# Kernel tuning notes

Measured on AMD Instinct MI355X. Metric: run time of the kernel, lower is better.

## Reference

```python
import jax, jax.numpy as jnp
import numpy as np

B, S, D, H = 2, 2048, 1024, 16
HD = D // H  # head_dim = 64


def setup_inputs() -> dict:
    key = jax.random.key(0)
    ks = jax.random.split(key, 12)
    sc = 1.0 / np.sqrt(D)
    return {
        "query": jax.random.normal(ks[0], (B, S, D), jnp.float32),
        "key_": jax.random.normal(ks[1], (B, S, D), jnp.float32),
        "value": jax.random.normal(ks[2], (B, S, D), jnp.float32),
        "mask": jax.random.randint(ks[3], (B, 1, S, S), 0, 2, jnp.int32),
        "Wq": jax.random.normal(ks[4], (D, D), jnp.float32) * sc,
        "bq": jnp.zeros((D,), jnp.float32),
        "Wk": jax.random.normal(ks[5], (D, D), jnp.float32) * sc,
        "bk": jnp.zeros((D,), jnp.float32),
        "Wv": jax.random.normal(ks[6], (D, D), jnp.float32) * sc,
        "bv": jnp.zeros((D,), jnp.float32),
        "Wo": jax.random.normal(ks[7], (D, D), jnp.float32) * sc,
        "bo": jnp.zeros((D,), jnp.float32),
    }


def _split(x):
    # [B, S, D] -> [B, H, S, HD]
    return x.reshape(B, S, H, HD).transpose(0, 2, 1, 3)


def reference(query, key_, value, mask, Wq, bq, Wk, bk, Wv, bv, Wo, bo):
    Q = _split(query @ Wq + bq)
    K = _split(key_ @ Wk + bk)
    V = _split(value @ Wv + bv)
    # scores: [B, H, Sq, Sk]
    scores = jnp.einsum("bhqd,bhkd->bhqk", Q, K) / jnp.sqrt(jnp.float32(HD))
    scores = jnp.where(mask == 0, jnp.float32(-1e9), scores)
    probs = jax.nn.softmax(scores, axis=-1)
    attn = jnp.einsum("bhqk,bhkd->bhqd", probs, V)
    out = attn.transpose(0, 2, 1, 3).reshape(B, S, D)
    return out @ Wo + bo
```

## Files before the change

kernel.cpp:

```cpp
#include <hip/hip_runtime.h>
#include <stdint.h>

typedef _Float16 f16;
typedef _Float16 f16x4 __attribute__((ext_vector_type(4)));
typedef _Float16 f16x8 __attribute__((ext_vector_type(8)));
typedef __fp16 hf16x2 __attribute__((ext_vector_type(2)));
typedef float f32x4 __attribute__((ext_vector_type(4)));
typedef float f32x16 __attribute__((ext_vector_type(16)));
typedef unsigned u32;
typedef unsigned uint2v __attribute__((ext_vector_type(2)));

static constexpr int Bb = 2, Ss = 2048, Dd = 1024, Hh = 16, HDd = 64;
static constexpr int M_ROWS = Bb * Ss;

static constexpr size_t OFF_WT  = 24ull << 20;
static constexpr size_t OFF_QKV = 32ull << 20;
static constexpr size_t OFF_ATT = 56ull << 20;
static constexpr size_t OFF_MB  = 64ull << 20;

__device__ __forceinline__ void gll16(const void* g, void* l) {
  __builtin_amdgcn_global_load_lds((__attribute__((address_space(1))) const void*)g,
                                   (__attribute__((address_space(3))) void*)l, 16, 0, 0);
}

__device__ __forceinline__ int lds_byte(int row, int slot) {
  return row * 128 + (((slot ^ (row & 7)) & 7) << 4);
}

__device__ __forceinline__ float ex2(float x) {
  float r; asm("v_exp_f32 %0, %1" : "=v"(r) : "v"(x)); return r;
}

union H2U { hf16x2 h; u32 u; };

__global__ __launch_bounds__(256) void prep(const int* __restrict__ mask,
                                            unsigned* __restrict__ bits,
                                            const float* __restrict__ wq,
                                            const float* __restrict__ wk,
                                            const float* __restrict__ wv,
                                            const float* __restrict__ wo,
                                            f16* __restrict__ wt) {
  const int bid = blockIdx.x;
  __shared__ float t[32][33];
  if (bid < 32768) {
    size_t i = (size_t)bid * 256 + threadIdx.x;
    int v = mask[i];
    unsigned long long bm = __ballot(v != 0);
    if ((threadIdx.x & 63) == 0) {
      size_t w = i >> 5;
      bits[w]     = (unsigned)bm;
      bits[w + 1] = (unsigned)(bm >> 32);
    }
  } else {
    const int wb = bid - 32768;
    const int z = wb >> 10, by = (wb >> 5) & 31, bx = wb & 31;
    const float* W = z == 0 ? wq : z == 1 ? wk : z == 2 ? wv : wo;
    f16* Wt = wt + (size_t)z * Dd * Dd;
    const int tx = threadIdx.x & 31, ty = threadIdx.x >> 5;
    const int k0 = by * 32, n0 = bx * 32;
    for (int i = 0; i < 32; i += 8) t[ty + i][tx] = W[(size_t)(k0 + ty + i) * Dd + n0 + tx];
    __syncthreads();
    for (int i = 0; i < 32; i += 8) Wt[(size_t)(n0 + ty + i) * Dd + k0 + tx] = (f16)t[tx][ty + i];
  }
}

__global__ __launch_bounds__(256) void gemm_qkv(const float* __restrict__ qin,
                                                const float* __restrict__ kin,
                                                const float* __restrict__ vin,
                                                const f16* __restrict__ Btbase,
                                                const float* __restrict__ b0,
                                                const float* __restrict__ b1,
                                                const float* __restrict__ b2,
                                                f16* __restrict__ Cbase) {
  constexpr int K = Dd, N = Dd;
  const int f = blockIdx.x;
  const int z = f >> 8, i = f & 255;
  const int xg = i & 7, sl = i >> 3;
  const int m0 = (xg * 4 + (sl >> 3)) * 128, n0 = (sl & 7) * 128;
  const float* A = z == 0 ? qin : z == 1 ? kin : vin;
  const f16* Bt = Btbase + (size_t)z * N * K;
  const float* bias = z == 0 ? b0 : z == 1 ? b1 : b2;

  __shared__ char smem[65536];
  const int tid = threadIdx.x, l = tid & 63, w = tid >> 6;
  const int li = l & 15, gq = l >> 4;
  const int wm = (w >> 1) * 64, wn = (w & 1) * 64;
  const int sr = l >> 3, ss = l & 7;
  const int scol = ((ss ^ sr) << 3);

  f32x4 acc[4][4];
  for (int mi = 0; mi < 4; mi++)
    for (int ni = 0; ni < 4; ni++) acc[mi][ni] = f32x4{0.f, 0.f, 0.f, 0.f};

  float4 a0[4], a1[4];
#pragma unroll
  for (int c = 0; c < 4; c++) {
    int chunk = w * 4 + c, r = chunk * 8 + sr;
    gll16(Bt + (size_t)(n0 + r) * K + scol, smem + 16384 + chunk * 1024);
    const float* src = A + (size_t)(m0 + r) * K + scol;
    a0[c] = *(const float4*)src; a1[c] = *(const float4*)(src + 4);
  }
#pragma unroll
  for (int c = 0; c < 4; c++) {
    int chunk = w * 4 + c;
    H2U h0, h1, h2, h3;
    h0.h = __builtin_amdgcn_cvt_pkrtz(a0[c].x, a0[c].y);
    h1.h = __builtin_amdgcn_cvt_pkrtz(a0[c].z, a0[c].w);
    h2.h = __builtin_amdgcn_cvt_pkrtz(a1[c].x, a1[c].y);
    h3.h = __builtin_amdgcn_cvt_pkrtz(a1[c].z, a1[c].w);
    union { u32 uu[4]; f16x8 v8; } pk;
    pk.uu[0] = h0.u; pk.uu[1] = h1.u; pk.uu[2] = h2.u; pk.uu[3] = h3.u;
    *(f16x8*)(smem + chunk * 1024 + l * 16) = pk.v8;
  }

  int cur = 0;
  for (int it = 0; it < 16; it++) {
    __syncthreads();
    char* Asc = smem + cur * 32768;
    char* Bsc = Asc + 16384;
    char* Asn = smem + (cur ^ 1) * 32768;
    char* Bsn = Asn + 16384;
    if (it < 15) {
      const int kn = (it + 1) * 64;
#pragma unroll
      for (int c = 0; c < 4; c++) {
        int chunk = w * 4 + c, r = chunk * 8 + sr;
        gll16(Bt + (size_t)(n0 + r) * K + kn + scol, Bsn + chunk * 1024);
        const float* src = A + (size_t)(m0 + r) * K + kn + scol;
        a0[c] = *(const float4*)src; a1[c] = *(const float4*)(src + 4);
      }
    }
#pragma unroll
    for (int ks = 0; ks < 2; ks++) {
      f16x8 af[4], bf[4];
#pragma unroll
      for (int ii = 0; ii < 4; ii++) {
        af[ii] = *(const f16x8*)(Asc + lds_byte(wm + ii * 16 + li, ks * 4 + gq));
        bf[ii] = *(const f16x8*)(Bsc + lds_byte(wn + ii * 16 + li, ks * 4 + gq));
      }
#pragma unroll
      for (int mi = 0; mi < 4; mi++)
#pragma unroll
        for (int ni = 0; ni < 4; ni++)
          acc[mi][ni] = __builtin_amdgcn_mfma_f32_16x16x32_f16(af[mi], bf[ni], acc[mi][ni], 0, 0, 0);
    }
    if (it < 15) {
#pragma unroll
      for (int c = 0; c < 4; c++) {
        int chunk = w * 4 + c;
        H2U h0, h1, h2, h3;
        h0.h = __builtin_amdgcn_cvt_pkrtz(a0[c].x, a0[c].y);
        h1.h = __builtin_amdgcn_cvt_pkrtz(a0[c].z, a0[c].w);
        h2.h = __builtin_amdgcn_cvt_pkrtz(a1[c].x, a1[c].y);
        h3.h = __builtin_amdgcn_cvt_pkrtz(a1[c].z, a1[c].w);
        union { u32 uu[4]; f16x8 v8; } pk;
        pk.uu[0] = h0.u; pk.uu[1] = h1.u; pk.uu[2] = h2.u; pk.uu[3] = h3.u;
        *(f16x8*)(Asn + chunk * 1024 + l * 16) = pk.v8;
      }
    }
    cur ^= 1;
  }

  const float scl = (z == 0) ? 0.18033688011112042f : 1.0f;
  if (z == 2) {
    f16* Vt = Cbase + (size_t)2 * M_ROWS * N;
#pragma unroll
    for (int mi = 0; mi < 4; mi++)
#pragma unroll
      for (int ni = 0; ni < 4; ni++) {
        const int col = n0 + wn + ni * 16 + li;
        const int r0  = m0 + wm + mi * 16 + gq * 4;
        const int bb_ = r0 >> 11, s = r0 & 2047;
        const float bv = bias[col];
        f16x4 pk;
#pragma unroll
        for (int j = 0; j < 4; j++) pk[j] = (f16)(acc[mi][ni][j] + bv);
        *(f16x4*)(Vt + ((size_t)(bb_ * Hh) << 17) + (size_t)col * Ss + s) = pk;
      }
  } else {
    for (int mi = 0; mi < 4; mi++)
      for (int ni = 0; ni < 4; ni++) {
        const int r0  = m0 + wm + mi * 16 + gq * 4;
        const int col = n0 + wn + ni * 16 + li;
        const float bb = bias[col];
#pragma unroll
        for (int j = 0; j < 4; j++) {
          float val = (acc[mi][ni][j] + bb) * scl;
          Cbase[(size_t)z * M_ROWS * N + (size_t)(r0 + j) * N + col] = (f16)val;
        }
      }
  }
}

__global__ __launch_bounds__(256) void gemm_out(const f16* __restrict__ A,
                                                const f16* __restrict__ Bt,
                                                const float* __restrict__ bias,
                                                float* __restrict__ C) {
  constexpr int K = Dd, N = Dd;
  const int f = blockIdx.x;
  const int xg = f & 7, sl = f >> 3;
  const int m0 = (xg * 4 + (sl >> 3)) * 128, n0 = (sl & 7) * 128;
  __shared__ char smem[65536];
  const int tid = threadIdx.x, l = tid & 63, w = tid >> 6;
  const int li = l & 15, gq = l >> 4;
  const int wm = (w >> 1) * 64, wn = (w & 1) * 64;
  const int sr = l >> 3, ss = l & 7;
  const int scol = ((ss ^ sr) << 3);

  f32x4 acc[4][4];
  for (int mi = 0; mi < 4; mi++)
    for (int ni = 0; ni < 4; ni++) acc[mi][ni] = f32x4{0.f, 0.f, 0.f, 0.f};

#pragma unroll
  for (int c = 0; c < 4; c++) {
    int chunk = w * 4 + c, r = chunk * 8 + sr;
    gll16(A  + (size_t)(m0 + r) * K + scol, smem + chunk * 1024);
    gll16(Bt + (size_t)(n0 + r) * K + scol, smem + 16384 + chunk * 1024);
  }

  int cur = 0;
  for (int it = 0; it < 16; it++) {
    __syncthreads();
    char* Asc = smem + cur * 32768;
    char* Bsc = Asc + 16384;
    if (it < 15) {
      char* Asn = smem + (cur ^ 1) * 32768;
      const int kn = (it + 1) * 64;
#pragma unroll
      for (int c = 0; c < 4; c++) {
        int chunk = w * 4 + c, r = chunk * 8 + sr;
        gll16(A  + (size_t)(m0 + r) * K + kn + scol, Asn + chunk * 1024);
        gll16(Bt + (size_t)(n0 + r) * K + kn + scol, Asn + 16384 + chunk * 1024);
      }
    }
#pragma unroll
    for (int ks = 0; ks < 2; ks++) {
      f16x8 af[4], bf[4];
#pragma unroll
      for (int ii = 0; ii < 4; ii++) {
        af[ii] = *(const f16x8*)(Asc + lds_byte(wm + ii * 16 + li, ks * 4 + gq));
        bf[ii] = *(const f16x8*)(Bsc + lds_byte(wn + ii * 16 + li, ks * 4 + gq));
      }
#pragma unroll
      for (int mi = 0; mi < 4; mi++)
#pragma unroll
        for (int ni = 0; ni < 4; ni++)
          acc[mi][ni] = __builtin_amdgcn_mfma_f32_16x16x32_f16(af[mi], bf[ni], acc[mi][ni], 0, 0, 0);
    }
    cur ^= 1;
  }

  for (int mi = 0; mi < 4; mi++)
    for (int ni = 0; ni < 4; ni++) {
      const int r0  = m0 + wm + mi * 16 + gq * 4;
      const int col = n0 + wn + ni * 16 + li;
      const float bb = bias[col];
#pragma unroll
      for (int j = 0; j < 4; j++)
        C[(size_t)(r0 + j) * N + col] = acc[mi][ni][j] + bb;
    }
}

__global__ __launch_bounds__(512, 4) void attn_fused(const f16* __restrict__ Qp,
                                                     const f16* __restrict__ Kp,
                                                     const f16* __restrict__ Vt,
                                                     const u32* __restrict__ mbits,
                                                     f16* __restrict__ outp) {
  const int flat = blockIdx.x;
  const int xcd = flat & 7, jj = flat >> 3;
  const int qt = jj & 15;
  const int hb = xcd * 4 + (jj >> 4);
  const int h = hb & 15, b = hb >> 4;

  const int tid = threadIdx.x, l = tid & 63, w = tid >> 6;
  const int lo = l & 31, hi = l >> 5;
  const int half = w >> 2, wsub = w & 3;
  const int q0 = qt * 128, wq = wsub * 32;

  __shared__ char smem[65536];
  char* hbase = smem + half * 32768;
  char* Qst = smem + 16384;

  const size_t qkbase = (size_t)b * Ss * Dd + (size_t)h * HDd;
  const f16* Vtb = Vt + (size_t)(b * Hh + h) * HDd * Ss;
  const int sr = l >> 3, ss = l & 7;
  const int scol = ((ss ^ sr) << 3);

  for (int c = 0; c < 2; c++) {
    int chunk = w * 2 + c, r = chunk * 8 + sr;
    gll16(Qp + qkbase + (size_t)(q0 + r) * Dd + scol, Qst + chunk * 1024);
  }
  const int kt0 = half * 16;
  for (int c = 0; c < 2; c++) {
    int chunk = wsub * 2 + c, r = chunk * 8 + sr;
    gll16(Kp + qkbase + (size_t)(kt0 * 64 + r) * Dd + scol, hbase + chunk * 1024);
    gll16(Vtb + (size_t)r * Ss + kt0 * 64 + scol, hbase + 8192 + chunk * 1024);
  }
  __syncthreads();

  f16x8 qf[4];
#pragma unroll
  for (int c = 0; c < 4; c++)
    qf[c] = *(const f16x8*)(Qst + lds_byte(wq + lo, 2 * c + hi));
  __syncthreads();

  f32x16 accO0 = {0}, accO1 = {0};
  float m_run = -1e30f, l_run = 0.f;
  const u32* mrow = mbits + (size_t)(b * Ss + q0 + wq + lo) * 64;

  for (int it = 0; it < 16; it++) {
    const int kt = kt0 + it;
    if (it) __syncthreads();
    char* bufc = hbase + (it & 1) * 16384;
    if (it < 15) {
      char* bufn = hbase + ((it + 1) & 1) * 16384;
      const int k0n = (kt + 1) * 64;
      for (int c = 0; c < 2; c++) {
        int chunk = wsub * 2 + c, r = chunk * 8 + sr;
        gll16(Kp + qkbase + (size_t)(k0n + r) * Dd + scol, bufn + chunk * 1024);
        gll16(Vtb + (size_t)r * Ss + k0n + scol, bufn + 8192 + chunk * 1024);
      }
    }
    const char* Kb = bufc;
    const char* Vb = bufc + 8192;

    f32x16 s0 = {0}, s1 = {0};
    __builtin_amdgcn_s_setprio(1);
#pragma unroll
    for (int c = 0; c < 4; c++) {
      f16x8 kf0 = *(const f16x8*)(Kb + lds_byte(lo, 2 * c + hi));
      f16x8 kf1 = *(const f16x8*)(Kb + lds_byte(32 + lo, 2 * c + hi));
      s0 = __builtin_amdgcn_mfma_f32_32x32x16_f16(kf0, qf[c], s0, 0, 0, 0);
      s1 = __builtin_amdgcn_mfma_f32_32x32x16_f16(kf1, qf[c], s1, 0, 0, 0);
    }
    __builtin_amdgcn_s_setprio(0);

    uint2v mw = *(const uint2v*)(mrow + kt * 2);
    u32 wa = mw.x >> (hi << 2);
    u32 wb = mw.y >> (hi << 2);

    float x0 = fmaxf(s0[0], s1[0]), x1 = fmaxf(s0[1], s1[1]);
    float x2 = fmaxf(s0[2], s1[2]), x3 = fmaxf(s0[3], s1[3]);
#pragma unroll
    for (int r = 4; r < 16; r += 4) {
      x0 = fmaxf(x0, fmaxf(s0[r],     s1[r]));
      x1 = fmaxf(x1, fmaxf(s0[r + 1], s1[r + 1]));
      x2 = fmaxf(x2, fmaxf(s0[r + 2], s1[r + 2]));
      x3 = fmaxf(x3, fmaxf(s0[r + 3], s1[r + 3]));
    }
    float pm = fmaxf(fmaxf(x0, x1), fmaxf(x2, x3));

    float mn;
    if (__all(pm <= m_run + 11.5f)) {
      mn = m_run;
    } else {
      pm = fmaxf(pm, __shfl_xor(pm, 32));
      mn = fmaxf(m_run, pm);
      const float so = ex2(m_run - mn);
      m_run = mn;
      l_run *= so;
      accO0 *= so; accO1 *= so;
    }

    float racc = 0.f;
#pragma unroll
    for (int r = 0; r < 16; r++) {
      const int kk = (r & 3) + 8 * (r >> 2);
      u32 ma = (u32)(((int)(wa << (31 - kk))) >> 31);
      u32 mb = (u32)(((int)(wb << (31 - kk))) >> 31);
      float e0 = __uint_as_float(__float_as_uint(ex2(s0[r] - mn)) & ma);
      float e1 = __uint_as_float(__float_as_uint(ex2(s1[r] - mn)) & mb);
      s0[r] = e0; s1[r] = e1;
      racc += e0 + e1;
    }
    l_run += racc;

    u32 pw[16];
#pragma unroll
    for (int j = 0; j < 8; j++) {
      H2U a, c;
      a.h = __builtin_amdgcn_cvt_pkrtz(s0[2 * j], s0[2 * j + 1]);
      c.h = __builtin_amdgcn_cvt_pkrtz(s1[2 * j], s1[2 * j + 1]);
      pw[j] = a.u; pw[8 + j] = c.u;
    }
#pragma unroll
    for (int c = 0; c < 4; c++) {
      asm volatile("v_permlane32_swap_b32 %0, %1" : "+v"(pw[4 * c]), "+v"(pw[4 * c + 2]));
      asm volatile("v_permlane32_swap_b32 %0, %1" : "+v"(pw[4 * c + 1]), "+v"(pw[4 * c + 3]));
    }

    __builtin_amdgcn_s_setprio(1);
#pragma unroll
    for (int c = 0; c < 4; c++) {
      union { u32 u[4]; f16x8 v; } pu;
      pu.u[0] = pw[4 * c]; pu.u[1] = pw[4 * c + 1];
      pu.u[2] = pw[4 * c + 2]; pu.u[3] = pw[4 * c + 3];
      f16x8 vf0 = *(const f16x8*)(Vb + lds_byte(lo, 2 * c + hi));
      f16x8 vf1 = *(const f16x8*)(Vb + lds_byte(32 + lo, 2 * c + hi));
      accO0 = __builtin_amdgcn_mfma_f32_32x32x16_f16(vf0, pu.v, accO0, 0, 0, 0);
      accO1 = __builtin_amdgcn_mfma_f32_32x32x16_f16(vf1, pu.v, accO1, 0, 0, 0);
    }
    __builtin_amdgcn_s_setprio(0);
  }

  __syncthreads();
  float* mg = (float*)smem;
  if (half == 1) {
    float* p = mg + (size_t)(wsub * 64 + l) * 35;
#pragma unroll
    for (int r = 0; r < 16; r++) { p[r] = accO0[r]; p[16 + r] = accO1[r]; }
    p[32] = m_run; p[33] = l_run;
  }
  __syncthreads();
  if (half == 1) return;

  const float* p = mg + (size_t)(wsub * 64 + l) * 35;
  const float mB = p[32], lB = p[33];
  const float m = fmaxf(m_run, mB);
  const float fA = ex2(m_run - m), fB = ex2(mB - m);
  float lmerged = l_run * fA + lB * fB;
#pragma unroll
  for (int r = 0; r < 16; r++) {
    accO0[r] = accO0[r] * fA + p[r] * fB;
    accO1[r] = accO1[r] * fA + p[16 + r] * fB;
  }
  const float lf = lmerged + __shfl_xor(lmerged, 32);
  const float inv = 1.0f / lf;

  char* Ot = smem + 40960 + wsub * 4096;
#pragma unroll
  for (int j = 0; j < 8; j++) {
    H2U pk;
    pk.h = __builtin_amdgcn_cvt_pkrtz(accO0[2 * j] * inv, accO0[2 * j + 1] * inv);
    int slot = (j >> 1);
    int addr = lo * 128 + (((slot ^ (lo & 7)) & 7) << 4) + 4 * (j & 1) + 8 * hi;
    *(u32*)(Ot + addr) = pk.u;
  }
#pragma unroll
  for (int j = 0; j < 8; j++) {
    H2U pk;
    pk.h = __builtin_amdgcn_cvt_pkrtz(accO1[2 * j] * inv, accO1[2 * j + 1] * inv);
    int slot = (j >> 1) + 4;
    int addr = lo * 128 + (((slot ^ (lo & 7)) & 7) << 4) + 4 * (j & 1) + 8 * hi;
    *(u32*)(Ot + addr) = pk.u;
  }
  asm volatile("s_waitcnt lgkmcnt(0)" ::: "memory");
  {
    const int q = l >> 1, halfq = l & 1;
    f16* gbase = outp + qkbase + (size_t)(q0 + wq + q) * Dd + halfq * 32;
#pragma unroll
    for (int c = 0; c < 4; c++) {
      int byte = q * 128 + ((((halfq * 4 + c) ^ (q & 7)) & 7) << 4);
      f16x8 v = *(const f16x8*)(Ot + byte);
      *(f16x8*)(gbase + c * 8) = v;
    }
  }
}

extern "C" void kernel_launch(void* const* d_in, const int* in_sizes, int n_in,
                              void* d_out, int out_size, void* d_ws, size_t ws_size,
                              hipStream_t stream) {
  const float* query = (const float*)d_in[0];
  const float* key_  = (const float*)d_in[1];
  const float* value = (const float*)d_in[2];
  const int*   mask  = (const int*)d_in[3];
  const float* Wq = (const float*)d_in[4];
  const float* bq = (const float*)d_in[5];
  const float* Wk = (const float*)d_in[6];
  const float* bk = (const float*)d_in[7];
  const float* Wv = (const float*)d_in[8];
  const float* bv = (const float*)d_in[9];
  const float* Wo = (const float*)d_in[10];
  const float* bo = (const float*)d_in[11];

  char* ws = (char*)d_ws;
  f16* Wt  = (f16*)(ws + OFF_WT);
  f16* QKV = (f16*)(ws + OFF_QKV);
  f16* ATT = (f16*)(ws + OFF_ATT);
  unsigned* MB = (unsigned*)(ws + OFF_MB);

  prep<<<dim3(32768 + 4096), 256, 0, stream>>>(mask, MB, Wq, Wk, Wv, Wo, Wt);
  gemm_qkv<<<dim3(768), 256, 0, stream>>>(query, key_, value, Wt, bq, bk, bv, QKV);
  attn_fused<<<dim3(512), 512, 0, stream>>>(QKV, QKV + (size_t)M_ROWS * Dd,
                                            QKV + 2 * (size_t)M_ROWS * Dd, MB, ATT);
  gemm_out<<<dim3(256), 256, 0, stream>>>(ATT, Wt + 3 * (size_t)Dd * Dd, bo, (float*)d_out);
}
```

Before: 138.1 us.

## Pre-convert QKV inputs to fp16 in prep and use async LDS loads in GEMM

The fp32 query/key/value activations are now converted to fp16 in the prep kernel and staged in workspace. The QKV GEMM then loads A tiles with global_load_lds, just like B, instead of doing register loads followed by a convert and LDS store. The block-to-tile mapping is also remapped so neighbouring blocks share A/B tiles for better L2 locality. The cost is an extra 24MB fp16 write plus reread through memory, in exchange for removing conversion work and register pressure from the GEMM main loop.

```diff
diff --git a/kernel.cpp b/kernel.cpp
--- a/kernel.cpp
+++ b/kernel.cpp
@@ -13,6 +13,7 @@
 static constexpr int Bb = 2, Ss = 2048, Dd = 1024, Hh = 16, HDd = 64;
 static constexpr int M_ROWS = Bb * Ss;
 
+static constexpr size_t OFF_X   = 0;
 static constexpr size_t OFF_WT  = 24ull << 20;
 static constexpr size_t OFF_QKV = 32ull << 20;
 static constexpr size_t OFF_ATT = 56ull << 20;
@@ -35,11 +36,15 @@
 
 __global__ __launch_bounds__(256) void prep(const int* __restrict__ mask,
                                             unsigned* __restrict__ bits,
+                                            const float* __restrict__ qin,
+                                            const float* __restrict__ kin,
+                                            const float* __restrict__ vin,
                                             const float* __restrict__ wq,
                                             const float* __restrict__ wk,
                                             const float* __restrict__ wv,
                                             const float* __restrict__ wo,
-                                            f16* __restrict__ wt) {
+                                            f16* __restrict__ wt,
+                                            f16* __restrict__ X) {
   const int bid = blockIdx.x;
   __shared__ float t[32][33];
   if (bid < 32768) {
@@ -51,7 +56,7 @@
       bits[w]     = (unsigned)bm;
       bits[w + 1] = (unsigned)(bm >> 32);
     }
-  } else {
+  } else if (bid < 36864) {
     const int wb = bid - 32768;
     const int z = wb >> 10, by = (wb >> 5) & 31, bx = wb & 31;
     const float* W = z == 0 ? wq : z == 1 ? wk : z == 2 ? wv : wo;
@@ -61,12 +66,20 @@
     for (int i = 0; i < 32; i += 8) t[ty + i][tx] = W[(size_t)(k0 + ty + i) * Dd + n0 + tx];
     __syncthreads();
     for (int i = 0; i < 32; i += 8) Wt[(size_t)(n0 + ty + i) * Dd + k0 + tx] = (f16)t[tx][ty + i];
-  }
-}
-
-__global__ __launch_bounds__(256) void gemm_qkv(const float* __restrict__ qin,
-                                                const float* __restrict__ kin,
-                                                const float* __restrict__ vin,
+  } else {
+    const int xb = bid - 36864;
+    const int zz = xb >> 12;
+    const float* src = zz == 0 ? qin : zz == 1 ? kin : vin;
+    f16* dst = X + (size_t)zz * M_ROWS * Dd;
+    size_t li = (size_t)(xb & 4095) * 256 + threadIdx.x;
+    float4 a = reinterpret_cast<const float4*>(src)[li];
+    f16x4 o;
+    o[0] = (f16)a.x; o[1] = (f16)a.y; o[2] = (f16)a.z; o[3] = (f16)a.w;
+    *reinterpret_cast<f16x4*>(dst + li * 4) = o;
+  }
+}
+
+__global__ __launch_bounds__(256) void gemm_qkv(const f16* __restrict__ Xbase,
                                                 const f16* __restrict__ Btbase,
                                                 const float* __restrict__ b0,
                                                 const float* __restrict__ b1,
@@ -74,10 +87,14 @@
                                                 f16* __restrict__ Cbase) {
   constexpr int K = Dd, N = Dd;
   const int f = blockIdx.x;
-  const int z = f >> 8, i = f & 255;
-  const int xg = i & 7, sl = i >> 3;
-  const int m0 = (xg * 4 + (sl >> 3)) * 128, n0 = (sl & 7) * 128;
-  const float* A = z == 0 ? qin : z == 1 ? kin : vin;
+  const int x = f & 7, j = f >> 3;
+  const int g = x * 12 + (j >> 3);
+  const int pos = j & 7;
+  const int z = g >> 5, gi = g & 31;
+  const int nq = gi >> 4, mp = gi & 15;
+  const int m0 = (mp * 2 + (pos & 1)) * 128;
+  const int n0 = (nq * 4 + (pos >> 1)) * 128;
+  const f16* A  = Xbase  + (size_t)z * M_ROWS * K;
   const f16* Bt = Btbase + (size_t)z * N * K;
   const float* bias = z == 0 ? b0 : z == 1 ? b1 : b2;
 
@@ -92,25 +109,11 @@
   for (int mi = 0; mi < 4; mi++)
     for (int ni = 0; ni < 4; ni++) acc[mi][ni] = f32x4{0.f, 0.f, 0.f, 0.f};
 
-  float4 a0[4], a1[4];
 #pragma unroll
   for (int c = 0; c < 4; c++) {
     int chunk = w * 4 + c, r = chunk * 8 + sr;
+    gll16(A  + (size_t)(m0 + r) * K + scol, smem + chunk * 1024);
     gll16(Bt + (size_t)(n0 + r) * K + scol, smem + 16384 + chunk * 1024);
-    const float* src = A + (size_t)(m0 + r) * K + scol;
-    a0[c] = *(const float4*)src; a1[c] = *(const float4*)(src + 4);
-  }
-#pragma unroll
-  for (int c = 0; c < 4; c++) {
-    int chunk = w * 4 + c;
-    H2U h0, h1, h2, h3;
-    h0.h = __builtin_amdgcn_cvt_pkrtz(a0[c].x, a0[c].y);
-    h1.h = __builtin_amdgcn_cvt_pkrtz(a0[c].z, a0[c].w);
-    h2.h = __builtin_amdgcn_cvt_pkrtz(a1[c].x, a1[c].y);
-    h3.h = __builtin_amdgcn_cvt_pkrtz(a1[c].z, a1[c].w);
-    union { u32 uu[4]; f16x8 v8; } pk;
-    pk.uu[0] = h0.u; pk.uu[1] = h1.u; pk.uu[2] = h2.u; pk.uu[3] = h3.u;
-    *(f16x8*)(smem + chunk * 1024 + l * 16) = pk.v8;
   }
 
   int cur = 0;
@@ -118,16 +121,14 @@
     __syncthreads();
     char* Asc = smem + cur * 32768;
     char* Bsc = Asc + 16384;
-    char* Asn = smem + (cur ^ 1) * 32768;
-    char* Bsn = Asn + 16384;
     if (it < 15) {
+      char* Asn = smem + (cur ^ 1) * 32768;
       const int kn = (it + 1) * 64;
 #pragma unroll
       for (int c = 0; c < 4; c++) {
         int chunk = w * 4 + c, r = chunk * 8 + sr;
-        gll16(Bt + (size_t)(n0 + r) * K + kn + scol, Bsn + chunk * 1024);
-        const float* src = A + (size_t)(m0 + r) * K + kn + scol;
-        a0[c] = *(const float4*)src; a1[c] = *(const float4*)(src + 4);
+        gll16(A  + (size_t)(m0 + r) * K + kn + scol, Asn + chunk * 1024);
+        gll16(Bt + (size_t)(n0 + r) * K + kn + scol, Asn + 16384 + chunk * 1024);
       }
     }
 #pragma unroll
@@ -143,20 +144,6 @@
 #pragma unroll
         for (int ni = 0; ni < 4; ni++)
           acc[mi][ni] = __builtin_amdgcn_mfma_f32_16x16x32_f16(af[mi], bf[ni], acc[mi][ni], 0, 0, 0);
-    }
-    if (it < 15) {
-#pragma unroll
-      for (int c = 0; c < 4; c++) {
-        int chunk = w * 4 + c;
-        H2U h0, h1, h2, h3;
-        h0.h = __builtin_amdgcn_cvt_pkrtz(a0[c].x, a0[c].y);
-        h1.h = __builtin_amdgcn_cvt_pkrtz(a0[c].z, a0[c].w);
-        h2.h = __builtin_amdgcn_cvt_pkrtz(a1[c].x, a1[c].y);
-        h3.h = __builtin_amdgcn_cvt_pkrtz(a1[c].z, a1[c].w);
-        union { u32 uu[4]; f16x8 v8; } pk;
-        pk.uu[0] = h0.u; pk.uu[1] = h1.u; pk.uu[2] = h2.u; pk.uu[3] = h3.u;
-        *(f16x8*)(Asn + chunk * 1024 + l * 16) = pk.v8;
-      }
     }
     cur ^= 1;
   }
@@ -174,7 +161,7 @@
         const float bv = bias[col];
         f16x4 pk;
 #pragma unroll
-        for (int j = 0; j < 4; j++) pk[j] = (f16)(acc[mi][ni][j] + bv);
+        for (int jj = 0; jj < 4; jj++) pk[jj] = (f16)(acc[mi][ni][jj] + bv);
         *(f16x4*)(Vt + ((size_t)(bb_ * Hh) << 17) + (size_t)col * Ss + s) = pk;
       }
   } else {
@@ -184,9 +171,9 @@
         const int col = n0 + wn + ni * 16 + li;
         const float bb = bias[col];
 #pragma unroll
-        for (int j = 0; j < 4; j++) {
-          float val = (acc[mi][ni][j] + bb) * scl;
-          Cbase[(size_t)z * M_ROWS * N + (size_t)(r0 + j) * N + col] = (f16)val;
+        for (int jj = 0; jj < 4; jj++) {
+          float val = (acc[mi][ni][jj] + bb) * scl;
+          Cbase[(size_t)z * M_ROWS * N + (size_t)(r0 + jj) * N + col] = (f16)val;
         }
       }
   }
@@ -256,8 +243,8 @@
       const int col = n0 + wn + ni * 16 + li;
       const float bb = bias[col];
 #pragma unroll
-      for (int j = 0; j < 4; j++)
-        C[(size_t)(r0 + j) * N + col] = acc[mi][ni][j] + bb;
+      for (int jj = 0; jj < 4; jj++)
+        C[(size_t)(r0 + jj) * N + col] = acc[mi][ni][jj] + bb;
     }
 }
 
@@ -377,11 +364,11 @@
 
     u32 pw[16];
 #pragma unroll
-    for (int j = 0; j < 8; j++) {
+    for (int j2 = 0; j2 < 8; j2++) {
       H2U a, c;
-      a.h = __builtin_amdgcn_cvt_pkrtz(s0[2 * j], s0[2 * j + 1]);
-      c.h = __builtin_amdgcn_cvt_pkrtz(s1[2 * j], s1[2 * j + 1]);
-      pw[j] = a.u; pw[8 + j] = c.u;
+      a.h = __builtin_amdgcn_cvt_pkrtz(s0[2 * j2], s0[2 * j2 + 1]);
+      c.h = __builtin_amdgcn_cvt_pkrtz(s1[2 * j2], s1[2 * j2 + 1]);
+      pw[j2] = a.u; pw[8 + j2] = c.u;
     }
 #pragma unroll
     for (int c = 0; c < 4; c++) {
@@ -429,19 +416,19 @@
 
   char* Ot = smem + 40960 + wsub * 4096;
 #pragma unroll
-  for (int j = 0; j < 8; j++) {
+  for (int j2 = 0; j2 < 8; j2++) {
     H2U pk;
-    pk.h = __builtin_amdgcn_cvt_pkrtz(accO0[2 * j] * inv, accO0[2 * j + 1] * inv);
-    int slot = (j >> 1);
-    int addr = lo * 128 + (((slot ^ (lo & 7)) & 7) << 4) + 4 * (j & 1) + 8 * hi;
+    pk.h = __builtin_amdgcn_cvt_pkrtz(accO0[2 * j2] * inv, accO0[2 * j2 + 1] * inv);
+    int slot = (j2 >> 1);
+    int addr = lo * 128 + (((slot ^ (lo & 7)) & 7) << 4) + 4 * (j2 & 1) + 8 * hi;
     *(u32*)(Ot + addr) = pk.u;
   }
 #pragma unroll
-  for (int j = 0; j < 8; j++) {
+  for (int j2 = 0; j2 < 8; j2++) {
     H2U pk;
-    pk.h = __builtin_amdgcn_cvt_pkrtz(accO1[2 * j] * inv, accO1[2 * j + 1] * inv);
-    int slot = (j >> 1) + 4;
-    int addr = lo * 128 + (((slot ^ (lo & 7)) & 7) << 4) + 4 * (j & 1) + 8 * hi;
+    pk.h = __builtin_amdgcn_cvt_pkrtz(accO1[2 * j2] * inv, accO1[2 * j2 + 1] * inv);
+    int slot = (j2 >> 1) + 4;
+    int addr = lo * 128 + (((slot ^ (lo & 7)) & 7) << 4) + 4 * (j2 & 1) + 8 * hi;
     *(u32*)(Ot + addr) = pk.u;
   }
   asm volatile("s_waitcnt lgkmcnt(0)" ::: "memory");
@@ -474,13 +461,15 @@
   const float* bo = (const float*)d_in[11];
 
   char* ws = (char*)d_ws;
+  f16* X   = (f16*)(ws + OFF_X);
   f16* Wt  = (f16*)(ws + OFF_WT);
   f16* QKV = (f16*)(ws + OFF_QKV);
   f16* ATT = (f16*)(ws + OFF_ATT);
   unsigned* MB = (unsigned*)(ws + OFF_MB);
 
-  prep<<<dim3(32768 + 4096), 256, 0, stream>>>(mask, MB, Wq, Wk, Wv, Wo, Wt);
-  gemm_qkv<<<dim3(768), 256, 0, stream>>>(query, key_, value, Wt, bq, bk, bv, QKV);
+  prep<<<dim3(32768 + 4096 + 12288), 256, 0, stream>>>(mask, MB, query, key_, value,
+                                                       Wq, Wk, Wv, Wo, Wt, X);
+  gemm_qkv<<<dim3(768), 256, 0, stream>>>(X, Wt, bq, bk, bv, QKV);
   attn_fused<<<dim3(512), 512, 0, stream>>>(QKV, QKV + (size_t)M_ROWS * Dd,
                                             QKV + 2 * (size_t)M_ROWS * Dd, MB, ATT);
   gemm_out<<<dim3(256), 256, 0, stream>>>(ATT, Wt + 3 * (size_t)Dd * Dd, bo, (float*)d_out);
```

Result: slower. 142.1 us (+2.9%).

## Drop split-K in attention: 4 waves per block iterate all key tiles

Applied to the files above, without the earlier changes.

The attention kernel previously used 8 waves per block, with two halves each processing half of the key tiles and merging partial softmax state through shared memory. Now each block has 4 waves that loop over all 32 key tiles, which removes the merge step and halves LDS use to 32KB. Q fragments are loaded straight from global memory instead of being staged through LDS. The aim is to cut merge and synchronisation overhead and raise occupancy, at the cost of a longer serial loop per wave and less parallelism within each block.

```diff
diff --git a/kernel.cpp b/kernel.cpp
--- a/kernel.cpp
+++ b/kernel.cpp
@@ -261,62 +261,50 @@
     }
 }
 
-__global__ __launch_bounds__(512, 4) void attn_fused(const f16* __restrict__ Qp,
+__global__ __launch_bounds__(256, 4) void attn_fused(const f16* __restrict__ Qp,
                                                      const f16* __restrict__ Kp,
                                                      const f16* __restrict__ Vt,
                                                      const u32* __restrict__ mbits,
                                                      f16* __restrict__ outp) {
-  const int flat = blockIdx.x;
-  const int xcd = flat & 7, jj = flat >> 3;
-  const int qt = jj & 15;
-  const int hb = xcd * 4 + (jj >> 4);
-  const int h = hb & 15, b = hb >> 4;
+  const int f = blockIdx.x;
+  const int xcd = f & 7, j = f >> 3;
+  const int qt = j & 15, g = j >> 4;
+  const int bh = xcd * 4 + g;
+  const int h = bh & 15, b = bh >> 4;
 
   const int tid = threadIdx.x, l = tid & 63, w = tid >> 6;
   const int lo = l & 31, hi = l >> 5;
-  const int half = w >> 2, wsub = w & 3;
-  const int q0 = qt * 128, wq = wsub * 32;
-
-  __shared__ char smem[65536];
-  char* hbase = smem + half * 32768;
-  char* Qst = smem + 16384;
-
+  const int q0 = qt * 128, wq = w * 32;
+
+  __shared__ char smem[32768];
   const size_t qkbase = (size_t)b * Ss * Dd + (size_t)h * HDd;
   const f16* Vtb = Vt + (size_t)(b * Hh + h) * HDd * Ss;
   const int sr = l >> 3, ss = l & 7;
   const int scol = ((ss ^ sr) << 3);
 
+  const f16* Qrow = Qp + qkbase + (size_t)(q0 + wq + lo) * Dd;
+  f16x8 qf[4];
+#pragma unroll
+  for (int c = 0; c < 4; c++) qf[c] = *(const f16x8*)(Qrow + 16 * c + 8 * hi);
+
   for (int c = 0; c < 2; c++) {
     int chunk = w * 2 + c, r = chunk * 8 + sr;
-    gll16(Qp + qkbase + (size_t)(q0 + r) * Dd + scol, Qst + chunk * 1024);
-  }
-  const int kt0 = half * 16;
-  for (int c = 0; c < 2; c++) {
-    int chunk = wsub * 2 + c, r = chunk * 8 + sr;
-    gll16(Kp + qkbase + (size_t)(kt0 * 64 + r) * Dd + scol, hbase + chunk * 1024);
-    gll16(Vtb + (size_t)r * Ss + kt0 * 64 + scol, hbase + 8192 + chunk * 1024);
-  }
-  __syncthreads();
-
-  f16x8 qf[4];
-#pragma unroll
-  for (int c = 0; c < 4; c++)
-    qf[c] = *(const f16x8*)(Qst + lds_byte(wq + lo, 2 * c + hi));
-  __syncthreads();
+    gll16(Kp + qkbase + (size_t)r * Dd + scol, smem + chunk * 1024);
+    gll16(Vtb + (size_t)r * Ss + scol, smem + 8192 + chunk * 1024);
+  }
 
   f32x16 accO0 = {0}, accO1 = {0};
   float m_run = -1e30f, l_run = 0.f;
   const u32* mrow = mbits + (size_t)(b * Ss + q0 + wq + lo) * 64;
 
-  for (int it = 0; it < 16; it++) {
-    const int kt = kt0 + it;
-    if (it) __syncthreads();
-    char* bufc = hbase + (it & 1) * 16384;
-    if (it < 15) {
-      char* bufn = hbase + ((it + 1) & 1) * 16384;
+  for (int kt = 0; kt < 32; kt++) {
+    __syncthreads();
+    char* bufc = smem + (kt & 1) * 16384;
+    if (kt < 31) {
+      char* bufn = smem + ((kt + 1) & 1) * 16384;
       const int k0n = (kt + 1) * 64;
       for (int c = 0; c < 2; c++) {
-        int chunk = wsub * 2 + c, r = chunk * 8 + sr;
+        int chunk = w * 2 + c, r = chunk * 8 + sr;
         gll16(Kp + qkbase + (size_t)(k0n + r) * Dd + scol, bufn + chunk * 1024);
         gll16(Vtb + (size_t)r * Ss + k0n + scol, bufn + 8192 + chunk * 1024);
       }
@@ -377,11 +365,11 @@
 
     u32 pw[16];
 #pragma unroll
-    for (int j = 0; j < 8; j++) {
+    for (int j2 = 0; j2 < 8; j2++) {
       H2U a, c;
-      a.h = __builtin_amdgcn_cvt_pkrtz(s0[2 * j], s0[2 * j + 1]);
-      c.h = __builtin_amdgcn_cvt_pkrtz(s1[2 * j], s1[2 * j + 1]);
-      pw[j] = a.u; pw[8 + j] = c.u;
+      a.h = __builtin_amdgcn_cvt_pkrtz(s0[2 * j2], s0[2 * j2 + 1]);
+      c.h = __builtin_amdgcn_cvt_pkrtz(s1[2 * j2], s1[2 * j2 + 1]);
+      pw[j2] = a.u; pw[8 + j2] = c.u;
     }
 #pragma unroll
     for (int c = 0; c < 4; c++) {
@@ -403,45 +391,25 @@
     __builtin_amdgcn_s_setprio(0);
   }
 
+  const float lf = l_run + __shfl_xor(l_run, 32);
+  const float inv = 1.0f / lf;
+
   __syncthreads();
-  float* mg = (float*)smem;
-  if (half == 1) {
-    float* p = mg + (size_t)(wsub * 64 + l) * 35;
-#pragma unroll
-    for (int r = 0; r < 16; r++) { p[r] = accO0[r]; p[16 + r] = accO1[r]; }
-    p[32] = m_run; p[33] = l_run;
-  }
-  __syncthreads();
-  if (half == 1) return;
-
-  const float* p = mg + (size_t)(wsub * 64 + l) * 35;
-  const float mB = p[32], lB = p[33];
-  const float m = fmaxf(m_run, mB);
-  const float fA = ex2(m_run - m), fB = ex2(mB - m);
-  float lmerged = l_run * fA + lB * fB;
-#pragma unroll
-  for (int r = 0; r < 16; r++) {
-    accO0[r] = accO0[r] * fA + p[r] * fB;
-    accO1[r] = accO1[r] * fA + p[16 + r] * fB;
-  }
-  const float lf = lmerged + __shfl_xor(lmerged, 32);
-  const float inv = 1.0f / lf;
-
-  char* Ot = smem + 40960 + wsub * 4096;
-#pragma unroll
-  for (int j = 0; j < 8; j++) {
+  char* Ot = smem + w * 4096;
+#pragma unroll
+  for (int j2 = 0; j2 < 8; j2++) {
     H2U pk;
-    pk.h = __builtin_amdgcn_cvt_pkrtz(accO0[2 * j] * inv, accO0[2 * j + 1] * inv);
-    int slot = (j >> 1);
-    int addr = lo * 128 + (((slot ^ (lo & 7)) & 7) << 4) + 4 * (j & 1) + 8 * hi;
+    pk.h = __builtin_amdgcn_cvt_pkrtz(accO0[2 * j2] * inv, accO0[2 * j2 + 1] * inv);
+    int slot = (j2 >> 1);
+    int addr = lo * 128 + (((slot ^ (lo & 7)) & 7) << 4) + 4 * (j2 & 1) + 8 * hi;
     *(u32*)(Ot + addr) = pk.u;
   }
 #pragma unroll
-  for (int j = 0; j < 8; j++) {
+  for (int j2 = 0; j2 < 8; j2++) {
     H2U pk;
-    pk.h = __builtin_amdgcn_cvt_pkrtz(accO1[2 * j] * inv, accO1[2 * j + 1] * inv);
-    int slot = (j >> 1) + 4;
-    int addr = lo * 128 + (((slot ^ (lo & 7)) & 7) << 4) + 4 * (j & 1) + 8 * hi;
+    pk.h = __builtin_amdgcn_cvt_pkrtz(accO1[2 * j2] * inv, accO1[2 * j2 + 1] * inv);
+    int slot = (j2 >> 1) + 4;
+    int addr = lo * 128 + (((slot ^ (lo & 7)) & 7) << 4) + 4 * (j2 & 1) + 8 * hi;
     *(u32*)(Ot + addr) = pk.u;
   }
   asm volatile("s_waitcnt lgkmcnt(0)" ::: "memory");
@@ -481,7 +449,7 @@
 
   prep<<<dim3(32768 + 4096), 256, 0, stream>>>(mask, MB, Wq, Wk, Wv, Wo, Wt);
   gemm_qkv<<<dim3(768), 256, 0, stream>>>(query, key_, value, Wt, bq, bk, bv, QKV);
-  attn_fused<<<dim3(512), 512, 0, stream>>>(QKV, QKV + (size_t)M_ROWS * Dd,
+  attn_fused<<<dim3(512), 256, 0, stream>>>(QKV, QKV + (size_t)M_ROWS * Dd,
                                             QKV + 2 * (size_t)M_ROWS * Dd, MB, ATT);
   gemm_out<<<dim3(256), 256, 0, stream>>>(ATT, Wt + 3 * (size_t)Dd * Dd, bo, (float*)d_out);
 }
```

Result: no change. 140.3 us (+1.6%).

## Deepen QKV GEMM pipeline to prefetch two K-tiles ahead with manual waitcnt

Applied to the files above, without the earlier changes.

Restructures the QKV projection GEMM main loop so global loads run two K-tiles ahead. The B tiles use a triple LDS buffer and the fp32 A tiles are held in two register sets. Explicit vmcnt/lgkmcnt waits and a single barrier per iteration replace the old double-buffered scheme, which loaded one tile ahead and converted after compute. This is meant to hide global memory latency better. In exchange, LDS use grows to 80KB, which may reduce occupancy, and register pressure rises from the doubled A staging.

```diff
diff --git a/kernel.cpp b/kernel.cpp
--- a/kernel.cpp
+++ b/kernel.cpp
@@ -81,7 +81,7 @@
   const f16* Bt = Btbase + (size_t)z * N * K;
   const float* bias = z == 0 ? b0 : z == 1 ? b1 : b2;
 
-  __shared__ char smem[65536];
+  __shared__ char smem[81920];
   const int tid = threadIdx.x, l = tid & 63, w = tid >> 6;
   const int li = l & 15, gq = l >> 4;
   const int wm = (w >> 1) * 64, wn = (w & 1) * 64;
@@ -92,44 +92,60 @@
   for (int mi = 0; mi < 4; mi++)
     for (int ni = 0; ni < 4; ni++) acc[mi][ni] = f32x4{0.f, 0.f, 0.f, 0.f};
 
-  float4 a0[4], a1[4];
-#pragma unroll
-  for (int c = 0; c < 4; c++) {
-    int chunk = w * 4 + c, r = chunk * 8 + sr;
-    gll16(Bt + (size_t)(n0 + r) * K + scol, smem + 16384 + chunk * 1024);
-    const float* src = A + (size_t)(m0 + r) * K + scol;
-    a0[c] = *(const float4*)src; a1[c] = *(const float4*)(src + 4);
-  }
-#pragma unroll
-  for (int c = 0; c < 4; c++) {
-    int chunk = w * 4 + c;
-    H2U h0, h1, h2, h3;
-    h0.h = __builtin_amdgcn_cvt_pkrtz(a0[c].x, a0[c].y);
-    h1.h = __builtin_amdgcn_cvt_pkrtz(a0[c].z, a0[c].w);
-    h2.h = __builtin_amdgcn_cvt_pkrtz(a1[c].x, a1[c].y);
-    h3.h = __builtin_amdgcn_cvt_pkrtz(a1[c].z, a1[c].w);
-    union { u32 uu[4]; f16x8 v8; } pk;
-    pk.uu[0] = h0.u; pk.uu[1] = h1.u; pk.uu[2] = h2.u; pk.uu[3] = h3.u;
-    *(f16x8*)(smem + chunk * 1024 + l * 16) = pk.v8;
-  }
-
-  int cur = 0;
-  for (int it = 0; it < 16; it++) {
-    __syncthreads();
-    char* Asc = smem + cur * 32768;
-    char* Bsc = Asc + 16384;
-    char* Asn = smem + (cur ^ 1) * 32768;
-    char* Bsn = Asn + 16384;
-    if (it < 15) {
-      const int kn = (it + 1) * 64;
+  float4 a0[2][4], a1[2][4];
+
+#pragma unroll
+  for (int t = 0; t < 2; t++) {
+    const int kt = t * 64;
+#pragma unroll
+    for (int c = 0; c < 4; c++) {
+      int chunk = w * 4 + c, r = chunk * 8 + sr;
+      gll16(Bt + (size_t)(n0 + r) * K + kt + scol, smem + 32768 + t * 16384 + chunk * 1024);
+      const float* src = A + (size_t)(m0 + r) * K + kt + scol;
+      a0[t][c] = *(const float4*)src;
+      a1[t][c] = *(const float4*)(src + 4);
+    }
+  }
+
+#pragma unroll
+  for (int t = 0; t < 16; t++) {
+    if (t < 15) asm volatile("s_waitcnt vmcnt(12)" ::: "memory");
+    else        asm volatile("s_waitcnt vmcnt(0)"  ::: "memory");
+
+    {
+      char* bufA = smem + (t & 1) * 16384;
+#pragma unroll
+      for (int c = 0; c < 4; c++) {
+        int chunk = w * 4 + c;
+        H2U h0, h1, h2, h3;
+        h0.h = __builtin_amdgcn_cvt_pkrtz(a0[t & 1][c].x, a0[t & 1][c].y);
+        h1.h = __builtin_amdgcn_cvt_pkrtz(a0[t & 1][c].z, a0[t & 1][c].w);
+        h2.h = __builtin_amdgcn_cvt_pkrtz(a1[t & 1][c].x, a1[t & 1][c].y);
+        h3.h = __builtin_amdgcn_cvt_pkrtz(a1[t & 1][c].z, a1[t & 1][c].w);
+        union { u32 uu[4]; f16x8 v8; } pk;
+        pk.uu[0] = h0.u; pk.uu[1] = h1.u; pk.uu[2] = h2.u; pk.uu[3] = h3.u;
+        *(f16x8*)(bufA + chunk * 1024 + l * 16) = pk.v8;
+      }
+    }
+    asm volatile("s_waitcnt lgkmcnt(0)" ::: "memory");
+    __builtin_amdgcn_s_barrier();
+
+    if (t + 2 < 16) {
+      const int tn = t + 2, kn = tn * 64;
 #pragma unroll
       for (int c = 0; c < 4; c++) {
         int chunk = w * 4 + c, r = chunk * 8 + sr;
-        gll16(Bt + (size_t)(n0 + r) * K + kn + scol, Bsn + chunk * 1024);
+        gll16(Bt + (size_t)(n0 + r) * K + kn + scol,
+              smem + 32768 + (tn % 3) * 16384 + chunk * 1024);
         const float* src = A + (size_t)(m0 + r) * K + kn + scol;
-        a0[c] = *(const float4*)src; a1[c] = *(const float4*)(src + 4);
-      }
-    }
+        a0[tn & 1][c] = *(const float4*)src;
+        a1[tn & 1][c] = *(const float4*)(src + 4);
+      }
+    }
+    __builtin_amdgcn_sched_barrier(0);
+
+    const char* Asc = smem + (t & 1) * 16384;
+    const char* Bsc = smem + 32768 + (t % 3) * 16384;
 #pragma unroll
     for (int ks = 0; ks < 2; ks++) {
       f16x8 af[4], bf[4];
@@ -144,21 +160,6 @@
         for (int ni = 0; ni < 4; ni++)
           acc[mi][ni] = __builtin_amdgcn_mfma_f32_16x16x32_f16(af[mi], bf[ni], acc[mi][ni], 0, 0, 0);
     }
-    if (it < 15) {
-#pragma unroll
-      for (int c = 0; c < 4; c++) {
-        int chunk = w * 4 + c;
-        H2U h0, h1, h2, h3;
-        h0.h = __builtin_amdgcn_cvt_pkrtz(a0[c].x, a0[c].y);
-        h1.h = __builtin_amdgcn_cvt_pkrtz(a0[c].z, a0[c].w);
-        h2.h = __builtin_amdgcn_cvt_pkrtz(a1[c].x, a1[c].y);
-        h3.h = __builtin_amdgcn_cvt_pkrtz(a1[c].z, a1[c].w);
-        union { u32 uu[4]; f16x8 v8; } pk;
-        pk.uu[0] = h0.u; pk.uu[1] = h1.u; pk.uu[2] = h2.u; pk.uu[3] = h3.u;
-        *(f16x8*)(Asn + chunk * 1024 + l * 16) = pk.v8;
-      }
-    }
-    cur ^= 1;
   }
 
   const float scl = (z == 0) ? 0.18033688011112042f : 1.0f;
```

New measurement: 133.3 us, median of 2. -3.5%, faster.
